# Kernel tuning notes

Hardware: AMD Instinct MI355X
Metric: run time of the kernel (lower is better)

Reference implementation:

```python
import jax, jax.numpy as jnp
import numpy as np

N_NODES = 20000
N_EDGES = 40000
N_GRAPHS = 500
D_IN = 32     # initial_dim_gcn
D_E = 16      # edge_dim_feature
H1 = 100      # hidden_dim_nn_1
H2 = 20       # hidden_dim_nn_2
F1 = 50       # hidden_dim_fcn_1


def setup_inputs() -> dict:
    key = jax.random.key(0)
    ks = jax.random.split(key, 16)
    s = lambda k, shp, fan: (jax.random.normal(k, shp, jnp.float32) / np.sqrt(fan)).astype(jnp.float32)
    return {
        "x": jax.random.normal(ks[0], (N_NODES, D_IN), jnp.float32),
        "edge_attr": jax.random.normal(ks[1], (N_EDGES, D_E), jnp.float32),
        "edge_index": jax.random.randint(ks[2], (2, N_EDGES), 0, N_NODES, jnp.int64),
        "batch": jnp.sort(jax.random.randint(ks[3], (N_NODES,), 0, N_GRAPHS, jnp.int64)),
        # NNConv layer 1: edge MLP Linear(D_E -> D_IN*H1), root weight, bias
        "nn1_W": s(ks[4], (D_E, D_IN * H1), D_E),
        "nn1_b": jnp.zeros((D_IN * H1,), jnp.float32),
        "root1": s(ks[5], (D_IN, H1), D_IN),
        "bias1": jnp.zeros((H1,), jnp.float32),
        # NNConv layer 2: edge MLP Linear(D_E -> H1*H2), root weight, bias
        "nn2_W": s(ks[6], (D_E, H1 * H2), D_E),
        "nn2_b": jnp.zeros((H1 * H2,), jnp.float32),
        "root2": s(ks[7], (H1, H2), H1),
        "bias2": jnp.zeros((H2,), jnp.float32),
        # FCN head
        "lin1_W": s(ks[8], (H2, F1), H2),
        "lin1_b": jnp.zeros((F1,), jnp.float32),
        "lin2_W": s(ks[9], (F1, 1), F1),
        "lin2_b": jnp.zeros((1,), jnp.float32),
    }


def _nnconv(x, src, dst, edge_attr, nnW, nnb, root, bias, d_in, d_out):
    # per-edge weight matrices: [E, d_in, d_out]
    theta = (edge_attr @ nnW + nnb).reshape(-1, d_in, d_out)
    # gather source features, per-edge matmul, scatter-add to targets
    msg = jnp.einsum('ei,eio->eo', x[src], theta)            # [E, d_out]
    agg = jax.ops.segment_sum(msg, dst, num_segments=x.shape[0])
    return agg + x @ root + bias


def reference(x, edge_attr, edge_index, batch,
              nn1_W, nn1_b, root1, bias1,
              nn2_W, nn2_b, root2, bias2,
              lin1_W, lin1_b, lin2_W, lin2_b):
    src, dst = edge_index[0], edge_index[1]  # PyG: message from j=src, aggregate at i=dst
    h = jax.nn.relu(_nnconv(x, src, dst, edge_attr, nn1_W, nn1_b, root1, bias1, D_IN, H1))
    h = jax.nn.relu(_nnconv(h, src, dst, edge_attr, nn2_W, nn2_b, root2, bias2, H1, H2))
    g = jax.ops.segment_sum(h, batch, num_segments=N_GRAPHS)  # sum-pool readout [G, H2]
    g = jax.nn.relu(g @ lin1_W + lin1_b)
    out = g @ lin2_W + lin2_b
    return out.reshape(-1)
```

## Files before the change

kernel.cpp:

```cpp
#include <hip/hip_runtime.h>
#include <hip/hip_bf16.h>
#include <hip/hip_fp16.h>

#define N_NODES 20000
#define N_EDGES 40000
#define N_GRAPHS 500
#define D_IN 32
#define D_E 16
#define H1 100
#define H2 20
#define F1 50

#define EB1 64
#define YNB 12
#define ET3 12

using h2f = __attribute__((ext_vector_type(2))) _Float16;
using h8f = __attribute__((ext_vector_type(8))) _Float16;
using f4  = __attribute__((ext_vector_type(4))) float;

__global__ __launch_bounds__(256) void prep_kernel(
    const float* __restrict__ nn1W, const float* __restrict__ nn1b,
    const float* __restrict__ nn2W, const float* __restrict__ nn2b,
    unsigned short* __restrict__ Wfrag1, unsigned short* __restrict__ Wfrag2,
    float* __restrict__ zbase)
{
  const int tid = blockIdx.x * 256 + threadIdx.x;
  if (tid < 544 * 112) {
    const int c  = tid / 3584;
    const int r  = tid % 3584;
    const int to = r / 512;
    const int l  = (r % 512) >> 3;
    const int j  = r & 7;
    const int i  = (l >> 4) * 8 + j;
    const int o  = to * 16 + (l & 15);
    float v = 0.f;
    if (o < H1) v = (c < 16) ? nn1W[c * (D_IN * H1) + i * H1 + o] : nn1b[i * H1 + o];
    _Float16 hv = (_Float16)v;
    Wfrag1[tid] = __builtin_bit_cast(unsigned short, hv);
  } else if (tid < 544 * 112 + 17 * 4096) {
    const int t2 = tid - 544 * 112;
    const int c  = t2 >> 12;
    const int q  = (t2 >> 10) & 3;
    const int to = (t2 >> 9) & 1;
    const int l  = (t2 >> 3) & 63;
    const int j  = t2 & 7;
    const int i  = q * 32 + (l >> 4) * 8 + j;
    const int o  = to * 16 + (l & 15);
    float v = 0.f;
    if (i < H1 && o < H2)
      v = (c < 16) ? nn2W[c * (H1 * H2) + i * H2 + o] : nn2b[i * H2 + o];
    _Float16 hv = (_Float16)v;
    Wfrag2[t2] = __builtin_bit_cast(unsigned short, hv);
  }
  float4* zp = (float4*)zbase;
  for (int i = tid; i < 602500; i += 512 * 256)
    zp[i] = make_float4(0.f, 0.f, 0.f, 0.f);
}

__global__ __launch_bounds__(256, 3) void edge1_kernel(
    const float* __restrict__ x, const float* __restrict__ ea,
    const int* __restrict__ eidx, const unsigned short* __restrict__ Wfrag,
    float* __restrict__ agg1)
{
  __shared__ uint4 Plds[4 * 64];
  __shared__ uint4 Blds[2][7 * 64];
  __shared__ int   sdst[EB1];

  const int t    = threadIdx.x;
  const int lane = t & 63;
  const int w    = t >> 6;
  const int e0   = blockIdx.x * EB1;

  const int e_loc = t >> 2;
  const int jg    = t & 3;
  const int src   = eidx[e0 + e_loc];

  h2f xh[4];
  {
    const float4* xp = (const float4*)&x[(size_t)src * D_IN + jg * 8];
    float4 v0 = xp[0], v1 = xp[1];
    float xf[8] = {v0.x, v0.y, v0.z, v0.w, v1.x, v1.y, v1.z, v1.w};
    #pragma unroll
    for (int j = 0; j < 4; ++j) {
      h2f p; p[0] = (_Float16)xf[2*j]; p[1] = (_Float16)xf[2*j+1]; xh[j] = p;
    }
  }
  _Float16 eh[17];
  {
    const float4* ep = (const float4*)&ea[(size_t)(e0 + e_loc) * D_E];
    float4 v0 = ep[0], v1 = ep[1], v2 = ep[2], v3 = ep[3];
    float ef[16] = {v0.x,v0.y,v0.z,v0.w, v1.x,v1.y,v1.z,v1.w,
                    v2.x,v2.y,v2.z,v2.w, v3.x,v3.y,v3.z,v3.w};
    #pragma unroll
    for (int k = 0; k < 16; ++k) eh[k] = (_Float16)ef[k];
    eh[16] = (_Float16)1.0f;
  }
  if (t < EB1) sdst[t] = eidx[N_EDGES + e0 + t];

  const uint4* __restrict__ Bf = (const uint4*)Wfrag;

  {
    uint4 s0 = Bf[t];
    uint4 s1;
    if (t < 192) s1 = Bf[256 + t];
    Blds[0][t] = s0;
    if (t < 192) Blds[0][256 + t] = s1;
  }
  __syncthreads();

  f4 acc[7];
  #pragma unroll
  for (int to = 0; to < 7; ++to) acc[to] = f4{0.f, 0.f, 0.f, 0.f};

  const int pslot = w * 64 + (e_loc & 15) + 16 * jg;

  #pragma unroll
  for (int c = 0; c < 17; ++c) {
    uint4 s0, s1;
    if (c < 16) {
      const uint4* bn = Bf + (c + 1) * 448;
      s0 = bn[t];
      if (t < 192) s1 = bn[256 + t];
    }

    h2f es; es[0] = eh[c]; es[1] = eh[c];
    unsigned int pk[4];
    #pragma unroll
    for (int j = 0; j < 4; ++j) {
      h2f pr = xh[j] * es;
      pk[j] = __builtin_bit_cast(unsigned int, pr);
    }
    Plds[pslot] = make_uint4(pk[0], pk[1], pk[2], pk[3]);

    uint4 a = Plds[w * 64 + lane];
    h8f A = __builtin_bit_cast(h8f, a);

    const uint4* bb = &Blds[c & 1][0];
    #pragma unroll
    for (int to = 0; to < 7; ++to) {
      h8f B = __builtin_bit_cast(h8f, bb[to * 64 + lane]);
      acc[to] = __builtin_amdgcn_mfma_f32_16x16x32_f16(A, B, acc[to], 0, 0, 0);
    }

    if (c < 16) {
      Blds[(c + 1) & 1][t] = s0;
      if (t < 192) Blds[(c + 1) & 1][256 + t] = s1;
    }
    __syncthreads();
  }

  const int col = lane & 15, rowg = lane >> 4;
  #pragma unroll
  for (int r = 0; r < 4; ++r) {
    const int el = w * 16 + rowg * 4 + r;
    const int d = sdst[el];
    float* ap = agg1 + (size_t)d * H1;
    #pragma unroll
    for (int to = 0; to < 7; ++to) {
      const int o = to * 16 + col;
      if (o < H1) unsafeAtomicAdd(&ap[o], acc[to][r]);
    }
  }
}

__global__ __launch_bounds__(256) void node1_kernel(
    const float* __restrict__ x, const float* __restrict__ agg1,
    const float* __restrict__ root1, const float* __restrict__ bias1,
    float* __restrict__ h1)
{
  __shared__ float sroot1[D_IN * H1];
  __shared__ float sxl[YNB * D_IN];
  const int t  = threadIdx.x;
  const int n0 = blockIdx.x * YNB;

  for (int idx = t; idx < 800; idx += 256)
    *(float4*)&sroot1[idx * 4] = *(const float4*)&root1[idx * 4];
  if (t < 96) {
    const int fo = t * 4;
    const int nn = fo >> 5;
    float4 v = make_float4(0.f, 0.f, 0.f, 0.f);
    if (n0 + nn < N_NODES) v = *(const float4*)&x[(size_t)n0 * D_IN + fo];
    *(float4*)&sxl[fo] = v;
  }
  __syncthreads();

  for (int idx = t; idx < YNB * H1; idx += 256) {
    const int nn = idx / H1, i = idx - nn * H1;
    const int n = n0 + nn;
    if (n < N_NODES) {
      float v = agg1[(size_t)n0 * H1 + idx] + bias1[i];
      #pragma unroll 8
      for (int d = 0; d < D_IN; ++d)
        v = fmaf(sxl[nn * D_IN + d], sroot1[d * H1 + i], v);
      h1[(size_t)n0 * H1 + idx] = fmaxf(v, 0.f);
    }
  }
}

__global__ __launch_bounds__(256, 3) void edge2m_kernel(
    const float* __restrict__ h1, const float* __restrict__ ea,
    const int* __restrict__ eidx, const unsigned short* __restrict__ Wfrag2,
    float* __restrict__ agg2)
{
  __shared__ uint4 Plds[4][4][64];
  __shared__ uint4 Blds[2][512];
  __shared__ int   sdst[EB1];

  const int t    = threadIdx.x;
  const int lane = t & 63;
  const int w    = t >> 6;
  const int e0   = blockIdx.x * EB1;

  const int e_loc = t >> 2;
  const int jg    = t & 3;
  const int m     = e_loc & 15;
  const int src   = eidx[e0 + e_loc];

  h2f xh[16];
  {
    float xf[32];
    const float* hp = &h1[(size_t)src * H1 + jg * 32];
    if (jg < 3) {
      #pragma unroll
      for (int q4 = 0; q4 < 8; ++q4) {
        float4 v = *(const float4*)&hp[q4 * 4];
        xf[q4*4+0] = v.x; xf[q4*4+1] = v.y; xf[q4*4+2] = v.z; xf[q4*4+3] = v.w;
      }
    } else {
      float4 v = *(const float4*)hp;
      xf[0] = v.x; xf[1] = v.y; xf[2] = v.z; xf[3] = v.w;
      #pragma unroll
      for (int ii = 4; ii < 32; ++ii) xf[ii] = 0.f;
    }
    #pragma unroll
    for (int j2 = 0; j2 < 16; ++j2) {
      h2f p; p[0] = (_Float16)xf[2*j2]; p[1] = (_Float16)xf[2*j2+1]; xh[j2] = p;
    }
  }
  _Float16 eh[17];
  {
    const float4* ep = (const float4*)&ea[(size_t)(e0 + e_loc) * D_E];
    float4 v0 = ep[0], v1 = ep[1], v2 = ep[2], v3 = ep[3];
    float ef[16] = {v0.x,v0.y,v0.z,v0.w, v1.x,v1.y,v1.z,v1.w,
                    v2.x,v2.y,v2.z,v2.w, v3.x,v3.y,v3.z,v3.w};
    #pragma unroll
    for (int k = 0; k < 16; ++k) eh[k] = (_Float16)ef[k];
    eh[16] = (_Float16)1.0f;
  }
  if (t < EB1) sdst[t] = eidx[N_EDGES + e0 + t];

  const uint4* __restrict__ Bf = (const uint4*)Wfrag2;

  {
    uint4 s0 = Bf[t];
    uint4 s1 = Bf[256 + t];
    Blds[0][t] = s0;
    Blds[0][256 + t] = s1;
  }
  {
    h2f es; es[0] = eh[0]; es[1] = eh[0];
    unsigned int pk[16];
    #pragma unroll
    for (int j2 = 0; j2 < 16; ++j2) {
      h2f pr = xh[j2] * es;
      pk[j2] = __builtin_bit_cast(unsigned int, pr);
    }
    #pragma unroll
    for (int oc = 0; oc < 4; ++oc)
      Plds[w][jg][16 * oc + m] = make_uint4(pk[4*oc], pk[4*oc+1], pk[4*oc+2], pk[4*oc+3]);
  }
  __syncthreads();

  f4 acc0 = f4{0.f, 0.f, 0.f, 0.f};
  f4 acc1 = f4{0.f, 0.f, 0.f, 0.f};

  #pragma unroll
  for (int c = 0; c < 17; ++c) {
    const int buf = c & 1;
    uint4 s0, s1;
    if (c < 16) {
      const uint4* bn = Bf + (c + 1) * 512;
      s0 = bn[t];
      s1 = bn[256 + t];
    }

    #pragma unroll
    for (int q = 0; q < 4; ++q) {
      uint4 a  = Plds[w][q][lane];
      uint4 b0 = Blds[buf][q * 128 + lane];
      uint4 b1 = Blds[buf][q * 128 + 64 + lane];
      h8f A  = __builtin_bit_cast(h8f, a);
      h8f B0 = __builtin_bit_cast(h8f, b0);
      h8f B1 = __builtin_bit_cast(h8f, b1);
      acc0 = __builtin_amdgcn_mfma_f32_16x16x32_f16(A, B0, acc0, 0, 0, 0);
      acc1 = __builtin_amdgcn_mfma_f32_16x16x32_f16(A, B1, acc1, 0, 0, 0);
    }

    if (c < 16) {
      h2f es; es[0] = eh[c + 1]; es[1] = eh[c + 1];
      unsigned int pk[16];
      #pragma unroll
      for (int j2 = 0; j2 < 16; ++j2) {
        h2f pr = xh[j2] * es;
        pk[j2] = __builtin_bit_cast(unsigned int, pr);
      }
      #pragma unroll
      for (int oc = 0; oc < 4; ++oc)
        Plds[w][jg][16 * oc + m] = make_uint4(pk[4*oc], pk[4*oc+1], pk[4*oc+2], pk[4*oc+3]);
      Blds[buf ^ 1][t] = s0;
      Blds[buf ^ 1][256 + t] = s1;
      __syncthreads();
    }
  }

  const int col = lane & 15, rowg = lane >> 4;
  #pragma unroll
  for (int r = 0; r < 4; ++r) {
    const int el = w * 16 + rowg * 4 + r;
    const int d  = sdst[el];
    float* ap = agg2 + (size_t)d * H2;
    unsafeAtomicAdd(&ap[col], acc0[r]);
    if (col < 4) unsafeAtomicAdd(&ap[16 + col], acc1[r]);
  }
}

__global__ __launch_bounds__(256) void node2_pool_kernel(
    const float* __restrict__ h1, const float* __restrict__ agg2,
    const float* __restrict__ root2, const float* __restrict__ bias2,
    const int* __restrict__ batch, float* __restrict__ g)
{
  __shared__ float sroot[H1 * H2];
  __shared__ float sv[ET3][H2];
  __shared__ int   sg[ET3];
  const int t  = threadIdx.x;
  const int n0 = blockIdx.x * ET3;

  for (int idx = t; idx < (H1 * H2) / 4; idx += 256)
    *(float4*)&sroot[idx * 4] = *(const float4*)&root2[idx * 4];
  if (t < ET3) {
    const int n = n0 + t;
    sg[t] = (n < N_NODES) ? batch[n] : -1;
  }
  __syncthreads();

  const int nl = t / H2, o = t % H2;
  const int n = n0 + nl;
  if (nl < ET3) {
    float v = 0.f;
    if (n < N_NODES) {
      v = agg2[(size_t)n * H2 + o] + bias2[o];
      const float* hr = &h1[(size_t)n * H1];
      #pragma unroll 5
      for (int i = 0; i < H1; i += 4) {
        const float4 hv = *(const float4*)&hr[i];
        v = fmaf(hv.x, sroot[(i    ) * H2 + o], v);
        v = fmaf(hv.y, sroot[(i + 1) * H2 + o], v);
        v = fmaf(hv.z, sroot[(i + 2) * H2 + o], v);
        v = fmaf(hv.w, sroot[(i + 3) * H2 + o], v);
      }
      v = fmaxf(v, 0.f);
    }
    sv[nl][o] = v;
  }
  __syncthreads();

  if (t < H2) {
    float run = 0.f;
    int cur = sg[0];
    #pragma unroll
    for (int r = 0; r < ET3; ++r) {
      const int gid = sg[r];
      if (gid != cur) {
        if (cur >= 0) unsafeAtomicAdd(&g[cur * H2 + t], run);
        run = 0.f; cur = gid;
      }
      run += sv[r][t];
    }
    if (cur >= 0) unsafeAtomicAdd(&g[cur * H2 + t], run);
  }
}

__global__ __launch_bounds__(64) void final_kernel(
    const float* __restrict__ g, const float* __restrict__ lin1W,
    const float* __restrict__ lin1b, const float* __restrict__ lin2W,
    const float* __restrict__ lin2b, float* __restrict__ out)
{
  const int gr = blockIdx.x;
  const int tt = threadIdx.x;
  float v = 0.f;
  if (tt < F1) {
    float s = lin1b[tt];
    #pragma unroll
    for (int o = 0; o < H2; ++o) s = fmaf(g[gr * H2 + o], lin1W[o * F1 + tt], s);
    v = fmaxf(s, 0.f) * lin2W[tt];
  }
  #pragma unroll
  for (int off = 32; off > 0; off >>= 1) v += __shfl_down(v, off, 64);
  if (tt == 0) out[gr] = v + lin2b[0];
}

extern "C" void kernel_launch(void* const* d_in, const int* in_sizes, int n_in,
                              void* d_out, int out_size, void* d_ws, size_t ws_size,
                              hipStream_t stream) {
  const float* x     = (const float*)d_in[0];
  const float* ea    = (const float*)d_in[1];
  const int*   eidx  = (const int*)d_in[2];
  const int*   batch = (const int*)d_in[3];
  const float* nn1W  = (const float*)d_in[4];
  const float* nn1b  = (const float*)d_in[5];
  const float* root1 = (const float*)d_in[6];
  const float* bias1 = (const float*)d_in[7];
  const float* nn2W  = (const float*)d_in[8];
  const float* nn2b  = (const float*)d_in[9];
  const float* root2 = (const float*)d_in[10];
  const float* bias2 = (const float*)d_in[11];
  const float* lin1W = (const float*)d_in[12];
  const float* lin1b = (const float*)d_in[13];
  const float* lin2W = (const float*)d_in[14];
  const float* lin2b = (const float*)d_in[15];
  float* out = (float*)d_out;

  float* ws   = (float*)d_ws;
  float* agg1 = ws;
  float* agg2 = agg1 + N_NODES * H1;
  float* g    = agg2 + N_NODES * H2;
  float* h1   = g    + N_GRAPHS * H2;
  unsigned short* Wfrag1 = (unsigned short*)(h1 + (size_t)N_NODES * H1);
  unsigned short* Wfrag2 = Wfrag1 + 61440;

  prep_kernel<<<512, 256, 0, stream>>>(nn1W, nn1b, nn2W, nn2b, Wfrag1, Wfrag2, agg1);
  edge1_kernel<<<N_EDGES / EB1, 256, 0, stream>>>(x, ea, eidx, Wfrag1, agg1);
  node1_kernel<<<(N_NODES + YNB - 1) / YNB, 256, 0, stream>>>(
      x, agg1, root1, bias1, h1);
  edge2m_kernel<<<N_EDGES / EB1, 256, 0, stream>>>(h1, ea, eidx, Wfrag2, agg2);
  node2_pool_kernel<<<(N_NODES + ET3 - 1) / ET3, 256, 0, stream>>>(
      h1, agg2, root2, bias2, batch, g);
  final_kernel<<<N_GRAPHS, 64, 0, stream>>>(g, lin1W, lin1b, lin2W, lin2b, out);
}
```

Baseline: 174.7 us.

## Fuse all six stages into one cooperative persistent kernel with grid syncs

Replaces the six separate kernel launches with a single cooperative mega-kernel that runs prep, edge1, node1, edge2, node2/pool and the final head as phases separated by grid.sync. Each phase uses grid-stride loops over the same tiles, and a union holds the per-phase shared memory. The aim is to remove per-launch overhead and inter-kernel gaps. In exchange, the grid is capped at 512 resident blocks, shared memory is sized to the largest phase, and grid-wide barriers add cost. A fallback to the multi-kernel path remains if the cooperative launch fails.

```diff
diff --git a/kernel.cpp b/kernel.cpp
--- a/kernel.cpp
+++ b/kernel.cpp
@@ -1,6 +1,8 @@
 #include <hip/hip_runtime.h>
-#include <hip/hip_bf16.h>
 #include <hip/hip_fp16.h>
+#include <hip/hip_cooperative_groups.h>
+
+namespace cg = cooperative_groups;
 
 #define N_NODES 20000
 #define N_EDGES 40000
@@ -14,10 +16,385 @@
 #define EB1 64
 #define YNB 12
 #define ET3 12
+#define NT_E 625
+#define NT_N 1667
 
 using h2f = __attribute__((ext_vector_type(2))) _Float16;
 using h8f = __attribute__((ext_vector_type(8))) _Float16;
 using f4  = __attribute__((ext_vector_type(4))) float;
+
+union SMemU {
+  struct { uint4 P[4 * 64]; uint4 B[2][7 * 64]; int sdst[EB1]; } e1;
+  struct { uint4 P[4][4][64]; uint4 B[2][512]; int sdst[EB1]; } e2;
+  struct { float sroot1[D_IN * H1]; float sxl[YNB * D_IN]; } n1;
+  struct { float sroot[H1 * H2]; float sv[ET3][H2]; int sg[ET3]; } n2;
+};
+
+__global__ __launch_bounds__(256, 2) void mega_kernel(
+    const float* __restrict__ x, const float* __restrict__ ea,
+    const int* __restrict__ eidx, const int* __restrict__ batch,
+    const float* __restrict__ nn1W, const float* __restrict__ nn1b,
+    const float* __restrict__ root1, const float* __restrict__ bias1,
+    const float* __restrict__ nn2W, const float* __restrict__ nn2b,
+    const float* __restrict__ root2, const float* __restrict__ bias2,
+    const float* __restrict__ lin1W, const float* __restrict__ lin1b,
+    const float* __restrict__ lin2W, const float* __restrict__ lin2b,
+    float* __restrict__ out, float* __restrict__ agg1, float* __restrict__ agg2,
+    float* __restrict__ g, float* __restrict__ h1,
+    unsigned short* __restrict__ Wfrag1, unsigned short* __restrict__ Wfrag2)
+{
+  cg::grid_group grid = cg::this_grid();
+  __shared__ SMemU sm;
+
+  const int t       = threadIdx.x;
+  const int lane    = t & 63;
+  const int w       = t >> 6;
+  const int gstride = gridDim.x * 256;
+
+  {
+    for (int tid = blockIdx.x * 256 + t; tid < 130560; tid += gstride) {
+      if (tid < 60928) {
+        const int c  = tid / 3584;
+        const int r  = tid % 3584;
+        const int to = r / 512;
+        const int l  = (r % 512) >> 3;
+        const int j  = r & 7;
+        const int i  = (l >> 4) * 8 + j;
+        const int o  = to * 16 + (l & 15);
+        float v = 0.f;
+        if (o < H1) v = (c < 16) ? nn1W[c * (D_IN * H1) + i * H1 + o] : nn1b[i * H1 + o];
+        _Float16 hv = (_Float16)v;
+        Wfrag1[tid] = __builtin_bit_cast(unsigned short, hv);
+      } else {
+        const int t2 = tid - 60928;
+        const int c  = t2 >> 12;
+        const int q  = (t2 >> 10) & 3;
+        const int to = (t2 >> 9) & 1;
+        const int l  = (t2 >> 3) & 63;
+        const int j  = t2 & 7;
+        const int i  = q * 32 + (l >> 4) * 8 + j;
+        const int o  = to * 16 + (l & 15);
+        float v = 0.f;
+        if (i < H1 && o < H2)
+          v = (c < 16) ? nn2W[c * (H1 * H2) + i * H2 + o] : nn2b[i * H2 + o];
+        _Float16 hv = (_Float16)v;
+        Wfrag2[t2] = __builtin_bit_cast(unsigned short, hv);
+      }
+    }
+    float4* zp = (float4*)agg1;
+    for (int i = blockIdx.x * 256 + t; i < 602500; i += gstride)
+      zp[i] = make_float4(0.f, 0.f, 0.f, 0.f);
+  }
+  grid.sync();
+
+  {
+    const uint4* __restrict__ Bf = (const uint4*)Wfrag1;
+    for (int tile = blockIdx.x; tile < NT_E; tile += gridDim.x) {
+      __syncthreads();
+      const int e0    = tile * EB1;
+      const int e_loc = t >> 2;
+      const int jg    = t & 3;
+      const int src   = eidx[e0 + e_loc];
+
+      h2f xh[4];
+      {
+        const float4* xp = (const float4*)&x[(size_t)src * D_IN + jg * 8];
+        float4 v0 = xp[0], v1 = xp[1];
+        float xf[8] = {v0.x, v0.y, v0.z, v0.w, v1.x, v1.y, v1.z, v1.w};
+        #pragma unroll
+        for (int j = 0; j < 4; ++j) {
+          h2f p; p[0] = (_Float16)xf[2*j]; p[1] = (_Float16)xf[2*j+1]; xh[j] = p;
+        }
+      }
+      _Float16 eh[17];
+      {
+        const float4* ep = (const float4*)&ea[(size_t)(e0 + e_loc) * D_E];
+        float4 v0 = ep[0], v1 = ep[1], v2 = ep[2], v3 = ep[3];
+        float ef[16] = {v0.x,v0.y,v0.z,v0.w, v1.x,v1.y,v1.z,v1.w,
+                        v2.x,v2.y,v2.z,v2.w, v3.x,v3.y,v3.z,v3.w};
+        #pragma unroll
+        for (int k = 0; k < 16; ++k) eh[k] = (_Float16)ef[k];
+        eh[16] = (_Float16)1.0f;
+      }
+      if (t < EB1) sm.e1.sdst[t] = eidx[N_EDGES + e0 + t];
+
+      {
+        uint4 s0 = Bf[t];
+        uint4 s1;
+        if (t < 192) s1 = Bf[256 + t];
+        sm.e1.B[0][t] = s0;
+        if (t < 192) sm.e1.B[0][256 + t] = s1;
+      }
+      __syncthreads();
+
+      f4 acc[7];
+      #pragma unroll
+      for (int to = 0; to < 7; ++to) acc[to] = f4{0.f, 0.f, 0.f, 0.f};
+
+      const int pslot = w * 64 + (e_loc & 15) + 16 * jg;
+
+      #pragma unroll
+      for (int c = 0; c < 17; ++c) {
+        uint4 s0, s1;
+        if (c < 16) {
+          const uint4* bn = Bf + (c + 1) * 448;
+          s0 = bn[t];
+          if (t < 192) s1 = bn[256 + t];
+        }
+
+        h2f es; es[0] = eh[c]; es[1] = eh[c];
+        unsigned int pk[4];
+        #pragma unroll
+        for (int j = 0; j < 4; ++j) {
+          h2f pr = xh[j] * es;
+          pk[j] = __builtin_bit_cast(unsigned int, pr);
+        }
+        sm.e1.P[pslot] = make_uint4(pk[0], pk[1], pk[2], pk[3]);
+
+        uint4 a = sm.e1.P[w * 64 + lane];
+        h8f A = __builtin_bit_cast(h8f, a);
+
+        const uint4* bb = &sm.e1.B[c & 1][0];
+        #pragma unroll
+        for (int to = 0; to < 7; ++to) {
+          h8f B = __builtin_bit_cast(h8f, bb[to * 64 + lane]);
+          acc[to] = __builtin_amdgcn_mfma_f32_16x16x32_f16(A, B, acc[to], 0, 0, 0);
+        }
+
+        if (c < 16) {
+          sm.e1.B[(c + 1) & 1][t] = s0;
+          if (t < 192) sm.e1.B[(c + 1) & 1][256 + t] = s1;
+        }
+        __syncthreads();
+      }
+
+      const int col = lane & 15, rowg = lane >> 4;
+      #pragma unroll
+      for (int r = 0; r < 4; ++r) {
+        const int el = w * 16 + rowg * 4 + r;
+        const int d = sm.e1.sdst[el];
+        float* ap = agg1 + (size_t)d * H1;
+        #pragma unroll
+        for (int to = 0; to < 7; ++to) {
+          const int o = to * 16 + col;
+          if (o < H1) unsafeAtomicAdd(&ap[o], acc[to][r]);
+        }
+      }
+    }
+  }
+  grid.sync();
+
+  {
+    for (int idx = t; idx < 800; idx += 256)
+      *(float4*)&sm.n1.sroot1[idx * 4] = *(const float4*)&root1[idx * 4];
+    for (int tile = blockIdx.x; tile < NT_N; tile += gridDim.x) {
+      __syncthreads();
+      const int n0 = tile * YNB;
+      if (t < 96) {
+        const int fo = t * 4;
+        const int nn = fo >> 5;
+        float4 v = make_float4(0.f, 0.f, 0.f, 0.f);
+        if (n0 + nn < N_NODES) v = *(const float4*)&x[(size_t)n0 * D_IN + fo];
+        *(float4*)&sm.n1.sxl[fo] = v;
+      }
+      __syncthreads();
+      for (int idx = t; idx < YNB * H1; idx += 256) {
+        const int nn = idx / H1, i = idx - nn * H1;
+        const int n = n0 + nn;
+        if (n < N_NODES) {
+          float v = agg1[(size_t)n0 * H1 + idx] + bias1[i];
+          #pragma unroll 8
+          for (int d = 0; d < D_IN; ++d)
+            v = fmaf(sm.n1.sxl[nn * D_IN + d], sm.n1.sroot1[d * H1 + i], v);
+          h1[(size_t)n0 * H1 + idx] = fmaxf(v, 0.f);
+        }
+      }
+    }
+  }
+  grid.sync();
+
+  {
+    const uint4* __restrict__ Bf = (const uint4*)Wfrag2;
+    for (int tile = blockIdx.x; tile < NT_E; tile += gridDim.x) {
+      __syncthreads();
+      const int e0    = tile * EB1;
+      const int e_loc = t >> 2;
+      const int jg    = t & 3;
+      const int m     = e_loc & 15;
+      const int src   = eidx[e0 + e_loc];
+
+      h2f xh[16];
+      {
+        float xf[32];
+        const float* hp = &h1[(size_t)src * H1 + jg * 32];
+        if (jg < 3) {
+          #pragma unroll
+          for (int q4 = 0; q4 < 8; ++q4) {
+            float4 v = *(const float4*)&hp[q4 * 4];
+            xf[q4*4+0] = v.x; xf[q4*4+1] = v.y; xf[q4*4+2] = v.z; xf[q4*4+3] = v.w;
+          }
+        } else {
+          float4 v = *(const float4*)hp;
+          xf[0] = v.x; xf[1] = v.y; xf[2] = v.z; xf[3] = v.w;
+          #pragma unroll
+          for (int ii = 4; ii < 32; ++ii) xf[ii] = 0.f;
+        }
+        #pragma unroll
+        for (int j2 = 0; j2 < 16; ++j2) {
+          h2f p; p[0] = (_Float16)xf[2*j2]; p[1] = (_Float16)xf[2*j2+1]; xh[j2] = p;
+        }
+      }
+      _Float16 eh[17];
+      {
+        const float4* ep = (const float4*)&ea[(size_t)(e0 + e_loc) * D_E];
+        float4 v0 = ep[0], v1 = ep[1], v2 = ep[2], v3 = ep[3];
+        float ef[16] = {v0.x,v0.y,v0.z,v0.w, v1.x,v1.y,v1.z,v1.w,
+                        v2.x,v2.y,v2.z,v2.w, v3.x,v3.y,v3.z,v3.w};
+        #pragma unroll
+        for (int k = 0; k < 16; ++k) eh[k] = (_Float16)ef[k];
+        eh[16] = (_Float16)1.0f;
+      }
+      if (t < EB1) sm.e2.sdst[t] = eidx[N_EDGES + e0 + t];
+
+      {
+        uint4 s0 = Bf[t];
+        uint4 s1 = Bf[256 + t];
+        sm.e2.B[0][t] = s0;
+        sm.e2.B[0][256 + t] = s1;
+      }
+      {
+        h2f es; es[0] = eh[0]; es[1] = eh[0];
+        unsigned int pk[16];
+        #pragma unroll
+        for (int j2 = 0; j2 < 16; ++j2) {
+          h2f pr = xh[j2] * es;
+          pk[j2] = __builtin_bit_cast(unsigned int, pr);
+        }
+        #pragma unroll
+        for (int oc = 0; oc < 4; ++oc)
+          sm.e2.P[w][jg][16 * oc + m] = make_uint4(pk[4*oc], pk[4*oc+1], pk[4*oc+2], pk[4*oc+3]);
+      }
+      __syncthreads();
+
+      f4 acc0 = f4{0.f, 0.f, 0.f, 0.f};
+      f4 acc1 = f4{0.f, 0.f, 0.f, 0.f};
+
+      #pragma unroll
+      for (int c = 0; c < 17; ++c) {
+        const int buf = c & 1;
+        uint4 s0, s1;
+        if (c < 16) {
+          const uint4* bn = Bf + (c + 1) * 512;
+          s0 = bn[t];
+          s1 = bn[256 + t];
+        }
+
+        #pragma unroll
+        for (int q = 0; q < 4; ++q) {
+          uint4 a  = sm.e2.P[w][q][lane];
+          uint4 b0 = sm.e2.B[buf][q * 128 + lane];
+          uint4 b1 = sm.e2.B[buf][q * 128 + 64 + lane];
+          h8f A  = __builtin_bit_cast(h8f, a);
+          h8f B0 = __builtin_bit_cast(h8f, b0);
+          h8f B1 = __builtin_bit_cast(h8f, b1);
+          acc0 = __builtin_amdgcn_mfma_f32_16x16x32_f16(A, B0, acc0, 0, 0, 0);
+          acc1 = __builtin_amdgcn_mfma_f32_16x16x32_f16(A, B1, acc1, 0, 0, 0);
+        }
+
+        if (c < 16) {
+          h2f es; es[0] = eh[c + 1]; es[1] = eh[c + 1];
+          unsigned int pk[16];
+          #pragma unroll
+          for (int j2 = 0; j2 < 16; ++j2) {
+            h2f pr = xh[j2] * es;
+            pk[j2] = __builtin_bit_cast(unsigned int, pr);
+          }
+          #pragma unroll
+          for (int oc = 0; oc < 4; ++oc)
+            sm.e2.P[w][jg][16 * oc + m] = make_uint4(pk[4*oc], pk[4*oc+1], pk[4*oc+2], pk[4*oc+3]);
+          sm.e2.B[buf ^ 1][t] = s0;
+          sm.e2.B[buf ^ 1][256 + t] = s1;
+          __syncthreads();
+        }
+      }
+
+      const int col = lane & 15, rowg = lane >> 4;
+      #pragma unroll
+      for (int r = 0; r < 4; ++r) {
+        const int el = w * 16 + rowg * 4 + r;
+        const int d  = sm.e2.sdst[el];
+        float* ap = agg2 + (size_t)d * H2;
+        unsafeAtomicAdd(&ap[col], acc0[r]);
+        if (col < 4) unsafeAtomicAdd(&ap[16 + col], acc1[r]);
+      }
+    }
+  }
+  grid.sync();
+
+  {
+    for (int idx = t; idx < 500; idx += 256)
+      *(float4*)&sm.n2.sroot[idx * 4] = *(const float4*)&root2[idx * 4];
+    for (int tile = blockIdx.x; tile < NT_N; tile += gridDim.x) {
+      __syncthreads();
+      const int n0 = tile * ET3;
+      if (t < ET3) {
+        const int n = n0 + t;
+        sm.n2.sg[t] = (n < N_NODES) ? batch[n] : -1;
+      }
+      const int nl = t / H2, o = t % H2;
+      const int n = n0 + nl;
+      if (nl < ET3) {
+        float v = 0.f;
+        if (n < N_NODES) {
+          v = agg2[(size_t)n * H2 + o] + bias2[o];
+          const float* hr = &h1[(size_t)n * H1];
+          #pragma unroll 5
+          for (int i = 0; i < H1; i += 4) {
+            const float4 hv = *(const float4*)&hr[i];
+            v = fmaf(hv.x, sm.n2.sroot[(i    ) * H2 + o], v);
+            v = fmaf(hv.y, sm.n2.sroot[(i + 1) * H2 + o], v);
+            v = fmaf(hv.z, sm.n2.sroot[(i + 2) * H2 + o], v);
+            v = fmaf(hv.w, sm.n2.sroot[(i + 3) * H2 + o], v);
+          }
+          v = fmaxf(v, 0.f);
+        }
+        sm.n2.sv[nl][o] = v;
+      }
+      __syncthreads();
+      if (t < H2) {
+        float run = 0.f;
+        int cur = sm.n2.sg[0];
+        #pragma unroll
+        for (int r = 0; r < ET3; ++r) {
+          const int gid = sm.n2.sg[r];
+          if (gid != cur) {
+            if (cur >= 0) unsafeAtomicAdd(&g[cur * H2 + t], run);
+            run = 0.f; cur = gid;
+          }
+          run += sm.n2.sv[r][t];
+        }
+        if (cur >= 0) unsafeAtomicAdd(&g[cur * H2 + t], run);
+      }
+    }
+  }
+  grid.sync();
+
+  {
+    for (int gb = blockIdx.x; gb < 125; gb += gridDim.x) {
+      const int gr = gb * 4 + w;
+      float v = 0.f;
+      if (lane < F1) {
+        float s = lin1b[lane];
+        #pragma unroll
+        for (int o = 0; o < H2; ++o) s = fmaf(g[gr * H2 + o], lin1W[o * F1 + lane], s);
+        v = fmaxf(s, 0.f) * lin2W[lane];
+      }
+      #pragma unroll
+      for (int off = 32; off > 0; off >>= 1) v += __shfl_down(v, off, 64);
+      if (lane == 0) out[gr] = v + lin2b[0];
+    }
+  }
+}
 
 __global__ __launch_bounds__(256) void prep_kernel(
     const float* __restrict__ nn1W, const float* __restrict__ nn1b,
@@ -99,7 +476,6 @@
   if (t < EB1) sdst[t] = eidx[N_EDGES + e0 + t];
 
   const uint4* __restrict__ Bf = (const uint4*)Wfrag;
-
   {
     uint4 s0 = Bf[t];
     uint4 s1;
@@ -123,7 +499,6 @@
       s0 = bn[t];
       if (t < 192) s1 = bn[256 + t];
     }
-
     h2f es; es[0] = eh[c]; es[1] = eh[c];
     unsigned int pk[4];
     #pragma unroll
@@ -142,7 +517,6 @@
       h8f B = __builtin_bit_cast(h8f, bb[to * 64 + lane]);
       acc[to] = __builtin_amdgcn_mfma_f32_16x16x32_f16(A, B, acc[to], 0, 0, 0);
     }
-
     if (c < 16) {
       Blds[(c + 1) & 1][t] = s0;
       if (t < 192) Blds[(c + 1) & 1][256 + t] = s1;
@@ -251,7 +625,6 @@
   if (t < EB1) sdst[t] = eidx[N_EDGES + e0 + t];
 
   const uint4* __restrict__ Bf = (const uint4*)Wfrag2;
-
   {
     uint4 s0 = Bf[t];
     uint4 s1 = Bf[256 + t];
@@ -284,7 +657,6 @@
       s0 = bn[t];
       s1 = bn[256 + t];
     }
-
     #pragma unroll
     for (int q = 0; q < 4; ++q) {
       uint4 a  = Plds[w][q][lane];
@@ -296,7 +668,6 @@
       acc0 = __builtin_amdgcn_mfma_f32_16x16x32_f16(A, B0, acc0, 0, 0, 0);
       acc1 = __builtin_amdgcn_mfma_f32_16x16x32_f16(A, B1, acc1, 0, 0, 0);
     }
-
     if (c < 16) {
       h2f es; es[0] = eh[c + 1]; es[1] = eh[c + 1];
       unsigned int pk[16];
@@ -429,12 +800,35 @@
   unsigned short* Wfrag1 = (unsigned short*)(h1 + (size_t)N_NODES * H1);
   unsigned short* Wfrag2 = Wfrag1 + 61440;
 
-  prep_kernel<<<512, 256, 0, stream>>>(nn1W, nn1b, nn2W, nn2b, Wfrag1, Wfrag2, agg1);
-  edge1_kernel<<<N_EDGES / EB1, 256, 0, stream>>>(x, ea, eidx, Wfrag1, agg1);
-  node1_kernel<<<(N_NODES + YNB - 1) / YNB, 256, 0, stream>>>(
-      x, agg1, root1, bias1, h1);
-  edge2m_kernel<<<N_EDGES / EB1, 256, 0, stream>>>(h1, ea, eidx, Wfrag2, agg2);
-  node2_pool_kernel<<<(N_NODES + ET3 - 1) / ET3, 256, 0, stream>>>(
-      h1, agg2, root2, bias2, batch, g);
-  final_kernel<<<N_GRAPHS, 64, 0, stream>>>(g, lin1W, lin1b, lin2W, lin2b, out);
+  int maxb = 0;
+  hipError_t qe = hipOccupancyMaxActiveBlocksPerMultiprocessor(
+      &maxb, reinterpret_cast<const void*>(&mega_kernel), 256, 0);
+  int nblk = 256;
+  if (qe == hipSuccess && maxb >= 1) {
+    int cap = maxb * 256;
+    nblk = cap < 512 ? cap : 512;
+  }
+
+  void* kargs[] = {
+      (void*)&x, (void*)&ea, (void*)&eidx, (void*)&batch,
+      (void*)&nn1W, (void*)&nn1b, (void*)&root1, (void*)&bias1,
+      (void*)&nn2W, (void*)&nn2b, (void*)&root2, (void*)&bias2,
+      (void*)&lin1W, (void*)&lin1b, (void*)&lin2W, (void*)&lin2b,
+      (void*)&out, (void*)&agg1, (void*)&agg2, (void*)&g, (void*)&h1,
+      (void*)&Wfrag1, (void*)&Wfrag2};
+
+  hipError_t le = hipLaunchCooperativeKernel(
+      reinterpret_cast<const void*>(&mega_kernel), dim3(nblk), dim3(256),
+      kargs, 0, stream);
+
+  if (le != hipSuccess) {
+    prep_kernel<<<512, 256, 0, stream>>>(nn1W, nn1b, nn2W, nn2b, Wfrag1, Wfrag2, agg1);
+    edge1_kernel<<<N_EDGES / EB1, 256, 0, stream>>>(x, ea, eidx, Wfrag1, agg1);
+    node1_kernel<<<(N_NODES + YNB - 1) / YNB, 256, 0, stream>>>(
+        x, agg1, root1, bias1, h1);
+    edge2m_kernel<<<N_EDGES / EB1, 256, 0, stream>>>(h1, ea, eidx, Wfrag2, agg2);
+    node2_pool_kernel<<<(N_NODES + ET3 - 1) / ET3, 256, 0, stream>>>(
+        h1, agg2, root2, bias2, batch, g);
+    final_kernel<<<N_GRAPHS, 64, 0, stream>>>(g, lin1W, lin1b, lin2W, lin2b, out);
+  }
 }
```

Result: slower. 375.9 us (+115.1%).

## Fold node1 root transform into prep and apply ReLU lazily in consumers

Applied to the files above, without the earlier changes.

Removes node1_kernel. The prep kernel now writes x@root1+bias1 straight into the aggregation buffer, which is no longer zeroed, and edge1 atomically adds messages on top of it. Edge2 and node2_pool apply ReLU when they read that buffer, so the separate h1 pass is gone. This saves one launch plus a full read and write of a 20000x100 array. In exchange, ReLU is recomputed at every gather, and prep does more work while zeroing less.

```diff
diff --git a/kernel.cpp b/kernel.cpp
--- a/kernel.cpp
+++ b/kernel.cpp
@@ -1,5 +1,4 @@
 #include <hip/hip_runtime.h>
-#include <hip/hip_bf16.h>
 #include <hip/hip_fp16.h>
 
 #define N_NODES 20000
@@ -22,10 +21,16 @@
 __global__ __launch_bounds__(256) void prep_kernel(
     const float* __restrict__ nn1W, const float* __restrict__ nn1b,
     const float* __restrict__ nn2W, const float* __restrict__ nn2b,
+    const float* __restrict__ root1, const float* __restrict__ bias1,
+    const float* __restrict__ x,
     unsigned short* __restrict__ Wfrag1, unsigned short* __restrict__ Wfrag2,
-    float* __restrict__ zbase)
+    float* __restrict__ pre1, float* __restrict__ zbase)
 {
-  const int tid = blockIdx.x * 256 + threadIdx.x;
+  __shared__ float sroot1[D_IN * H1];
+  __shared__ float sxl[YNB * D_IN];
+  const int t   = threadIdx.x;
+  const int tid = blockIdx.x * 256 + t;
+
   if (tid < 544 * 112) {
     const int c  = tid / 3584;
     const int r  = tid % 3584;
@@ -53,9 +58,39 @@
     _Float16 hv = (_Float16)v;
     Wfrag2[t2] = __builtin_bit_cast(unsigned short, hv);
   }
-  float4* zp = (float4*)zbase;
-  for (int i = tid; i < 602500; i += 512 * 256)
-    zp[i] = make_float4(0.f, 0.f, 0.f, 0.f);
+
+  {
+    float4* zp = (float4*)zbase;
+    for (int i = tid; i < 102500; i += 512 * 256)
+      zp[i] = make_float4(0.f, 0.f, 0.f, 0.f);
+  }
+
+  for (int idx = t; idx < 800; idx += 256)
+    *(float4*)&sroot1[idx * 4] = *(const float4*)&root1[idx * 4];
+
+  for (int tile = blockIdx.x; tile < 1667; tile += 512) {
+    const int n0 = tile * YNB;
+    __syncthreads();
+    if (t < 96) {
+      const int fo = t * 4;
+      const int nn = fo >> 5;
+      float4 v = make_float4(0.f, 0.f, 0.f, 0.f);
+      if (n0 + nn < N_NODES) v = *(const float4*)&x[(size_t)n0 * D_IN + fo];
+      *(float4*)&sxl[fo] = v;
+    }
+    __syncthreads();
+    for (int idx = t; idx < YNB * H1; idx += 256) {
+      const int nn = idx / H1, i = idx - nn * H1;
+      const int n = n0 + nn;
+      if (n < N_NODES) {
+        float v = bias1[i];
+        #pragma unroll 8
+        for (int d = 0; d < D_IN; ++d)
+          v = fmaf(sxl[nn * D_IN + d], sroot1[d * H1 + i], v);
+        pre1[(size_t)n0 * H1 + idx] = v;
+      }
+    }
+  }
 }
 
 __global__ __launch_bounds__(256, 3) void edge1_kernel(
@@ -99,7 +134,6 @@
   if (t < EB1) sdst[t] = eidx[N_EDGES + e0 + t];
 
   const uint4* __restrict__ Bf = (const uint4*)Wfrag;
-
   {
     uint4 s0 = Bf[t];
     uint4 s1;
@@ -123,7 +157,6 @@
       s0 = bn[t];
       if (t < 192) s1 = bn[256 + t];
     }
-
     h2f es; es[0] = eh[c]; es[1] = eh[c];
     unsigned int pk[4];
     #pragma unroll
@@ -142,7 +175,6 @@
       h8f B = __builtin_bit_cast(h8f, bb[to * 64 + lane]);
       acc[to] = __builtin_amdgcn_mfma_f32_16x16x32_f16(A, B, acc[to], 0, 0, 0);
     }
-
     if (c < 16) {
       Blds[(c + 1) & 1][t] = s0;
       if (t < 192) Blds[(c + 1) & 1][256 + t] = s1;
@@ -164,42 +196,8 @@
   }
 }
 
-__global__ __launch_bounds__(256) void node1_kernel(
-    const float* __restrict__ x, const float* __restrict__ agg1,
-    const float* __restrict__ root1, const float* __restrict__ bias1,
-    float* __restrict__ h1)
-{
-  __shared__ float sroot1[D_IN * H1];
-  __shared__ float sxl[YNB * D_IN];
-  const int t  = threadIdx.x;
-  const int n0 = blockIdx.x * YNB;
-
-  for (int idx = t; idx < 800; idx += 256)
-    *(float4*)&sroot1[idx * 4] = *(const float4*)&root1[idx * 4];
-  if (t < 96) {
-    const int fo = t * 4;
-    const int nn = fo >> 5;
-    float4 v = make_float4(0.f, 0.f, 0.f, 0.f);
-    if (n0 + nn < N_NODES) v = *(const float4*)&x[(size_t)n0 * D_IN + fo];
-    *(float4*)&sxl[fo] = v;
-  }
-  __syncthreads();
-
-  for (int idx = t; idx < YNB * H1; idx += 256) {
-    const int nn = idx / H1, i = idx - nn * H1;
-    const int n = n0 + nn;
-    if (n < N_NODES) {
-      float v = agg1[(size_t)n0 * H1 + idx] + bias1[i];
-      #pragma unroll 8
-      for (int d = 0; d < D_IN; ++d)
-        v = fmaf(sxl[nn * D_IN + d], sroot1[d * H1 + i], v);
-      h1[(size_t)n0 * H1 + idx] = fmaxf(v, 0.f);
-    }
-  }
-}
-
 __global__ __launch_bounds__(256, 3) void edge2m_kernel(
-    const float* __restrict__ h1, const float* __restrict__ ea,
+    const float* __restrict__ pre1, const float* __restrict__ ea,
     const int* __restrict__ eidx, const unsigned short* __restrict__ Wfrag2,
     float* __restrict__ agg2)
 {
@@ -220,16 +218,18 @@
   h2f xh[16];
   {
     float xf[32];
-    const float* hp = &h1[(size_t)src * H1 + jg * 32];
+    const float* hp = &pre1[(size_t)src * H1 + jg * 32];
     if (jg < 3) {
       #pragma unroll
       for (int q4 = 0; q4 < 8; ++q4) {
         float4 v = *(const float4*)&hp[q4 * 4];
-        xf[q4*4+0] = v.x; xf[q4*4+1] = v.y; xf[q4*4+2] = v.z; xf[q4*4+3] = v.w;
+        xf[q4*4+0] = fmaxf(v.x, 0.f); xf[q4*4+1] = fmaxf(v.y, 0.f);
+        xf[q4*4+2] = fmaxf(v.z, 0.f); xf[q4*4+3] = fmaxf(v.w, 0.f);
       }
     } else {
       float4 v = *(const float4*)hp;
-      xf[0] = v.x; xf[1] = v.y; xf[2] = v.z; xf[3] = v.w;
+      xf[0] = fmaxf(v.x, 0.f); xf[1] = fmaxf(v.y, 0.f);
+      xf[2] = fmaxf(v.z, 0.f); xf[3] = fmaxf(v.w, 0.f);
       #pragma unroll
       for (int ii = 4; ii < 32; ++ii) xf[ii] = 0.f;
     }
@@ -251,7 +251,6 @@
   if (t < EB1) sdst[t] = eidx[N_EDGES + e0 + t];
 
   const uint4* __restrict__ Bf = (const uint4*)Wfrag2;
-
   {
     uint4 s0 = Bf[t];
     uint4 s1 = Bf[256 + t];
@@ -284,7 +283,6 @@
       s0 = bn[t];
       s1 = bn[256 + t];
     }
-
     #pragma unroll
     for (int q = 0; q < 4; ++q) {
       uint4 a  = Plds[w][q][lane];
@@ -296,7 +294,6 @@
       acc0 = __builtin_amdgcn_mfma_f32_16x16x32_f16(A, B0, acc0, 0, 0, 0);
       acc1 = __builtin_amdgcn_mfma_f32_16x16x32_f16(A, B1, acc1, 0, 0, 0);
     }
-
     if (c < 16) {
       h2f es; es[0] = eh[c + 1]; es[1] = eh[c + 1];
       unsigned int pk[16];
@@ -326,7 +323,7 @@
 }
 
 __global__ __launch_bounds__(256) void node2_pool_kernel(
-    const float* __restrict__ h1, const float* __restrict__ agg2,
+    const float* __restrict__ pre1, const float* __restrict__ agg2,
     const float* __restrict__ root2, const float* __restrict__ bias2,
     const int* __restrict__ batch, float* __restrict__ g)
 {
@@ -350,14 +347,14 @@
     float v = 0.f;
     if (n < N_NODES) {
       v = agg2[(size_t)n * H2 + o] + bias2[o];
-      const float* hr = &h1[(size_t)n * H1];
+      const float* hr = &pre1[(size_t)n * H1];
       #pragma unroll 5
       for (int i = 0; i < H1; i += 4) {
         const float4 hv = *(const float4*)&hr[i];
-        v = fmaf(hv.x, sroot[(i    ) * H2 + o], v);
-        v = fmaf(hv.y, sroot[(i + 1) * H2 + o], v);
-        v = fmaf(hv.z, sroot[(i + 2) * H2 + o], v);
-        v = fmaf(hv.w, sroot[(i + 3) * H2 + o], v);
+        v = fmaf(fmaxf(hv.x, 0.f), sroot[(i    ) * H2 + o], v);
+        v = fmaf(fmaxf(hv.y, 0.f), sroot[(i + 1) * H2 + o], v);
+        v = fmaf(fmaxf(hv.z, 0.f), sroot[(i + 2) * H2 + o], v);
+        v = fmaf(fmaxf(hv.w, 0.f), sroot[(i + 3) * H2 + o], v);
       }
       v = fmaxf(v, 0.f);
     }
@@ -422,19 +419,18 @@
   float* out = (float*)d_out;
 
   float* ws   = (float*)d_ws;
-  float* agg1 = ws;
-  float* agg2 = agg1 + N_NODES * H1;
+  float* pre1 = ws;
+  float* agg2 = pre1 + N_NODES * H1;
   float* g    = agg2 + N_NODES * H2;
   float* h1   = g    + N_GRAPHS * H2;
   unsigned short* Wfrag1 = (unsigned short*)(h1 + (size_t)N_NODES * H1);
   unsigned short* Wfrag2 = Wfrag1 + 61440;
 
-  prep_kernel<<<512, 256, 0, stream>>>(nn1W, nn1b, nn2W, nn2b, Wfrag1, Wfrag2, agg1);
-  edge1_kernel<<<N_EDGES / EB1, 256, 0, stream>>>(x, ea, eidx, Wfrag1, agg1);
-  node1_kernel<<<(N_NODES + YNB - 1) / YNB, 256, 0, stream>>>(
-      x, agg1, root1, bias1, h1);
-  edge2m_kernel<<<N_EDGES / EB1, 256, 0, stream>>>(h1, ea, eidx, Wfrag2, agg2);
+  prep_kernel<<<512, 256, 0, stream>>>(nn1W, nn1b, nn2W, nn2b, root1, bias1, x,
+                                       Wfrag1, Wfrag2, pre1, agg2);
+  edge1_kernel<<<N_EDGES / EB1, 256, 0, stream>>>(x, ea, eidx, Wfrag1, pre1);
+  edge2m_kernel<<<N_EDGES / EB1, 256, 0, stream>>>(pre1, ea, eidx, Wfrag2, agg2);
   node2_pool_kernel<<<(N_NODES + ET3 - 1) / ET3, 256, 0, stream>>>(
-      h1, agg2, root2, bias2, batch, g);
+      pre1, agg2, root2, bias2, batch, g);
   final_kernel<<<N_GRAPHS, 64, 0, stream>>>(g, lin1W, lin1b, lin2W, lin2b, out);
 }
```

New measurement: 174.5 us. About the same (-0.1%).
